# Kernel tuning notes

Hardware: AMD Instinct MI355X
Metric: run time of the kernel (lower is better)

## Reference

```python
import jax, jax.numpy as jnp
import numpy as np

ADAPTERS = 40   # adapter_num, hard-coded by range(40) and tsv 40x40
CAPS = 3        # num_capsules
CLASS_DIM = 200 # MAX_SEQ
IN_CH = CAPS * CLASS_DIM  # 600
B = 256
D = 768
NUM_ITERS = 3


def squash(v, axis=-1):
    sq = jnp.sum(v * v, axis=axis, keepdims=True)
    return (sq / (1.0 + sq)) * v / jnp.sqrt(sq)


def setup_inputs() -> dict:
    key = jax.random.key(0)
    k0, k1, k2, k3, k4 = jax.random.split(key, 5)
    x = jax.random.normal(k0, (B, ADAPTERS, IN_CH), jnp.float32)
    s = jax.random.uniform(k1, (1,), jnp.float32) * 4.0 + 1.0  # gate temperature
    route_weights = jax.random.normal(k2, (ADAPTERS, CAPS, IN_CH, CLASS_DIM), jnp.float32)
    larger_w = jax.random.normal(k3, (D, CAPS), jnp.float32) * 0.1  # Linear(3,768) weight [out,in]
    larger_b = jnp.zeros((D,), jnp.float32)
    elarger = jax.random.normal(k4, (ADAPTERS, D), jnp.float32)     # Embedding(40,768)
    tsv = jnp.tril(jnp.ones((ADAPTERS, ADAPTERS), jnp.float32))
    return {"t": 20, "x": x, "s": s, "route_weights": route_weights,
            "larger_w": larger_w, "larger_b": larger_b, "elarger": elarger, "tsv": tsv}


def reference(t, x, s, route_weights, larger_w, larger_b, elarger, tsv):
    bz = x.shape[0]
    # per-adapter small matmuls, batched: priors[n,b,k,d] = sum_c x[b,k,c] * W[k,n,c,d]
    priors = jnp.einsum('bkc,kncd->nbkd', x, route_weights)[:, :, :, None, :]  # [3,B,40,1,200]
    tsv_t = tsv[t]                                   # [40]
    mask = jnp.where(tsv_t == 0, -10000.0, 0.0)      # [40]
    tsv_b = tsv_t[None, None, :, None, None]
    mask_b = mask[None, None, :, None, None]
    logits = jnp.zeros_like(priors)
    vote = None
    for i in range(NUM_ITERS):
        logits = logits * tsv_b + mask_b
        probs = jax.nn.softmax(logits, axis=2)       # my_softmax over adapter dim
        vote = jnp.sum(probs * priors, axis=2, keepdims=True)   # [3,B,1,1,200]
        out = squash(vote, axis=-1)
        if i != NUM_ITERS - 1:
            logits = logits + jnp.sum(priors * out, axis=-1, keepdims=True)
    # torch's .view(bz, length, -1) on a [3,B,1,1,200] tensor: row-major reinterpretation
    h = vote.reshape(bz, CLASS_DIM, CAPS)            # [B,200,3]
    h = h @ larger_w.T + larger_b                    # [B,200,768]
    g = jax.nn.sigmoid(s * elarger[t])               # [768] (broadcast of [1]*[768])
    return h * g
```

## Files before the change

### kernel.cpp

```cpp
#include <hip/hip_runtime.h>
#include <hip/hip_bf16.h>

#define ADAPTERS 40
#define CAPS 3
#define IN_CH 600
#define BSZ 256
#define DCLS 200
#define DMODEL 768

typedef __attribute__((ext_vector_type(8))) short short8;
typedef __attribute__((ext_vector_type(4))) float f32x4;
typedef __attribute__((ext_vector_type(4))) float f4v;

#define RP 40
#define NCHUNK 19

__device__ __forceinline__ void split2(float f0, float f1,
                                       unsigned& hi, unsigned& lo) {
    unsigned u0 = __float_as_uint(f0), u1 = __float_as_uint(f1);
    unsigned h0 = u0 & 0xFFFF0000u, h1 = u1 & 0xFFFF0000u;
    hi = (u0 >> 16) | h1;
    float l0 = f0 - __uint_as_float(h0);
    float l1 = f1 - __uint_as_float(h1);
    lo = (__float_as_uint(l0) >> 16) | (__float_as_uint(l1) & 0xFFFF0000u);
}

__global__ __launch_bounds__(512) void k1_priors(
    const float* __restrict__ x,
    const float* __restrict__ rw,
    const float* __restrict__ tsv,
    const int* __restrict__ t_p,
    float* __restrict__ priors)
{
    int kk = blockIdx.z;
    int t = t_p[0];
    if (tsv[t * ADAPTERS + kk] == 0.0f) return;

    int b0 = blockIdx.x * 128;
    int j0 = blockIdx.y * 128;

    __shared__ __align__(16) unsigned short Ahi[128 * RP];
    __shared__ __align__(16) unsigned short Alo[128 * RP];
    __shared__ __align__(16) unsigned short Bhi[128 * RP];
    __shared__ __align__(16) unsigned short Blo[128 * RP];

    int tid = threadIdx.x;
    int lane = tid & 63, w = tid >> 6;
    int lm = lane & 15, lq = lane >> 4;
    int m0w = (w & 1) * 64;
    int n0w = (w >> 1) * 32;

    int a_bi = tid >> 2;
    int a_ci0 = (tid & 3) * 8;
    const float* a_row = x + ((size_t)(b0 + a_bi) * ADAPTERS + kk) * IN_CH;
    int b_jj = tid >> 2;
    int b_ci0 = (tid & 3) * 8;
    int j = j0 + b_jj;
    bool jvalid = (j < CAPS * DCLS);
    int cap = (j >= 2 * DCLS) ? 2 : ((j >= DCLS) ? 1 : 0);
    int d = j - cap * DCLS;
    const float* b_base = rw + ((size_t)(kk * 3 + cap) * IN_CH) * DCLS + d;

    f32x4 acc[4][2];
    #pragma unroll
    for (int mt = 0; mt < 4; mt++)
        #pragma unroll
        for (int nt = 0; nt < 2; nt++)
            acc[mt][nt] = (f32x4){0.f, 0.f, 0.f, 0.f};

    float4 ax[2];
    float  bx[8];

    {
        int c0 = 0;
        #pragma unroll
        for (int q = 0; q < 2; q++) {
            int c = c0 + a_ci0 + q * 4;
            ax[q] = (c + 4 <= IN_CH) ? *(const float4*)(a_row + c)
                                     : make_float4(0.f, 0.f, 0.f, 0.f);
        }
        #pragma unroll
        for (int i = 0; i < 8; i++) {
            int c = c0 + b_ci0 + i;
            bx[i] = (jvalid && c < IN_CH) ? b_base[(size_t)c * DCLS] : 0.f;
        }
    }

    for (int ch = 0; ch < NCHUNK; ch++) {
        unsigned ahi[4], alo[4], bhi[4], blo[4];
        split2(ax[0].x, ax[0].y, ahi[0], alo[0]);
        split2(ax[0].z, ax[0].w, ahi[1], alo[1]);
        split2(ax[1].x, ax[1].y, ahi[2], alo[2]);
        split2(ax[1].z, ax[1].w, ahi[3], alo[3]);
        #pragma unroll
        for (int p = 0; p < 4; p++)
            split2(bx[2 * p], bx[2 * p + 1], bhi[p], blo[p]);

        __syncthreads();
        {
            *(uint4*)((unsigned*)&Ahi[a_bi * RP + a_ci0]) =
                make_uint4(ahi[0], ahi[1], ahi[2], ahi[3]);
            *(uint4*)((unsigned*)&Alo[a_bi * RP + a_ci0]) =
                make_uint4(alo[0], alo[1], alo[2], alo[3]);
            *(uint4*)((unsigned*)&Bhi[b_jj * RP + b_ci0]) =
                make_uint4(bhi[0], bhi[1], bhi[2], bhi[3]);
            *(uint4*)((unsigned*)&Blo[b_jj * RP + b_ci0]) =
                make_uint4(blo[0], blo[1], blo[2], blo[3]);
        }
        __syncthreads();

        if (ch + 1 < NCHUNK) {
            int c0 = (ch + 1) * 32;
            #pragma unroll
            for (int q = 0; q < 2; q++) {
                int c = c0 + a_ci0 + q * 4;
                ax[q] = (c + 4 <= IN_CH) ? *(const float4*)(a_row + c)
                                         : make_float4(0.f, 0.f, 0.f, 0.f);
            }
            #pragma unroll
            for (int i = 0; i < 8; i++) {
                int c = c0 + b_ci0 + i;
                bx[i] = (jvalid && c < IN_CH) ? b_base[(size_t)c * DCLS] : 0.f;
            }
        }

        short8 Afh[4], Afl[4];
        #pragma unroll
        for (int mt = 0; mt < 4; mt++) {
            int row = m0w + mt * 16 + lm;
            Afh[mt] = *(const short8*)&Ahi[row * RP + lq * 8];
            Afl[mt] = *(const short8*)&Alo[row * RP + lq * 8];
        }
        #pragma unroll
        for (int nt = 0; nt < 2; nt++) {
            int row = n0w + nt * 16 + lm;
            short8 bh = *(const short8*)&Bhi[row * RP + lq * 8];
            short8 bl = *(const short8*)&Blo[row * RP + lq * 8];
            #pragma unroll
            for (int mt = 0; mt < 4; mt++) {
                acc[mt][nt] = __builtin_amdgcn_mfma_f32_16x16x32_bf16(
                    bh, Afh[mt], acc[mt][nt], 0, 0, 0);
                acc[mt][nt] = __builtin_amdgcn_mfma_f32_16x16x32_bf16(
                    bl, Afh[mt], acc[mt][nt], 0, 0, 0);
                acc[mt][nt] = __builtin_amdgcn_mfma_f32_16x16x32_bf16(
                    bh, Afl[mt], acc[mt][nt], 0, 0, 0);
            }
        }
    }

    #pragma unroll
    for (int nt = 0; nt < 2; nt++) {
        int jc = j0 + n0w + nt * 16 + lq * 4;
        if (jc >= CAPS * DCLS) continue;
        int capc = (jc >= 2 * DCLS) ? 2 : ((jc >= DCLS) ? 1 : 0);
        int dc = jc - capc * DCLS;
        #pragma unroll
        for (int mt = 0; mt < 4; mt++) {
            int b = b0 + m0w + mt * 16 + lm;
            float* dst = priors +
                ((size_t)(capc * BSZ + b) * ADAPTERS + kk) * DCLS + dc;
            *(f4v*)dst = *(f4v*)&acc[mt][nt];
        }
    }
}

__global__ __launch_bounds__(256) void k2_route(
    const float* __restrict__ priors,
    const float* __restrict__ tsv,
    const int* __restrict__ t_p,
    float* __restrict__ vote)
{
    int nb = blockIdx.x;
    int n = nb >> 8, b = nb & 255;
    int tid = threadIdx.x;
    int lane = tid & 63, wid = tid >> 6;

    __shared__ float Ps[ADAPTERS * DCLS];
    __shared__ float vout[DCLS];
    __shared__ float act[ADAPTERS];
    __shared__ float a_s[ADAPTERS];
    __shared__ float probs_s[ADAPTERS];
    __shared__ int   klist[ADAPTERS];
    __shared__ int   nact_s;
    __shared__ float red[4];
    __shared__ float scl;

    int t = t_p[0];
    if (tid < ADAPTERS) {
        act[tid] = tsv[t * ADAPTERS + tid];
        a_s[tid] = 0.0f;
    }
    __syncthreads();

    if (tid == 0) {
        int c = 0;
        for (int k = 0; k < ADAPTERS; k++)
            if (act[k] != 0.0f) klist[c++] = k;
        nact_s = c;
    }

    {
        const float4* pb4 = (const float4*)
            (priors + (size_t)(n * BSZ + b) * ADAPTERS * DCLS);
        float4* Ps4 = (float4*)Ps;
        for (int i4 = tid; i4 < ADAPTERS * (DCLS / 4); i4 += 256) {
            int k = i4 / (DCLS / 4);
            if (act[k] != 0.0f) Ps4[i4] = pb4[i4];
        }
    }
    __syncthreads();

    int nact = nact_s;
    float cnt = (float)nact;

    int td = tid;
    float v = 0.0f;
    if (td < DCLS) {
        for (int ki = 0; ki < nact; ki++)
            v += Ps[klist[ki] * DCLS + td];
        v /= cnt;
    }

    for (int it = 0; it < 3; it++) {
        if (it > 0) {
            if (wid == 0) {
                bool on = (lane < ADAPTERS) && (act[lane] != 0.f);
                float val = on ? a_s[lane] : -3.0e38f;
                float m = val;
                for (int off = 32; off; off >>= 1)
                    m = fmaxf(m, __shfl_down(m, off));
                m = __shfl(m, 0);
                float e = on ? expf(val - m) : 0.f;
                float ssum = e;
                for (int off = 32; off; off >>= 1)
                    ssum += __shfl_down(ssum, off);
                ssum = __shfl(ssum, 0);
                if (lane < ADAPTERS) probs_s[lane] = e / ssum;
            }
            __syncthreads();
            v = 0.0f;
            if (td < DCLS) {
                for (int ki = 0; ki < nact; ki++) {
                    int k = klist[ki];
                    v += probs_s[k] * Ps[k * DCLS + td];
                }
            }
        }
        if (it == 2) break;

        float vv = (td < DCLS) ? v * v : 0.f;
        for (int off = 32; off; off >>= 1) vv += __shfl_down(vv, off);
        if (lane == 0) red[wid] = vv;
        __syncthreads();
        if (tid == 0) {
            float sq = red[0] + red[1] + red[2] + red[3];
            scl = sqrtf(sq) / (1.0f + sq);
        }
        __syncthreads();
        if (td < DCLS) vout[td] = v * scl;
        __syncthreads();

        for (int ki = wid; ki < nact; ki += 4) {
            int k = klist[ki];
            const float* row = Ps + k * DCLS;
            float p = row[lane] * vout[lane]
                    + row[lane + 64] * vout[lane + 64]
                    + row[lane + 128] * vout[lane + 128];
            if (lane < DCLS - 192) p += row[lane + 192] * vout[lane + 192];
            for (int off = 32; off; off >>= 1) p += __shfl_down(p, off);
            if (lane == 0) a_s[k] += p;
        }
        __syncthreads();
    }

    if (td < DCLS) vote[(size_t)n * BSZ * DCLS + b * DCLS + td] = v;
}

__global__ __launch_bounds__(256) void k3_out(
    const float* __restrict__ vote,
    const float* __restrict__ s_p,
    const float* __restrict__ lw,
    const float* __restrict__ lb,
    const float* __restrict__ el,
    const int* __restrict__ t_p,
    float* __restrict__ out)
{
    __shared__ float vs[192];
    int tid = threadIdx.x;
    int r0 = blockIdx.x * 64;
    if (tid < 192) vs[tid] = vote[r0 * 3 + tid];

    int lane = tid & 63;
    int ty = tid >> 6;
    int j = blockIdx.y * 256 + lane * 4;

    int t = t_p[0];
    float s = s_p[0];
    float4 e4  = *(const float4*)(el + (size_t)t * DMODEL + j);
    float4 lb4 = *(const float4*)(lb + j);
    const float4* lw4 = (const float4*)(lw + (size_t)j * 3);
    float4 w0 = lw4[0], w1 = lw4[1], w2 = lw4[2];
    float ga = 1.0f / (1.0f + expf(-s * e4.x));
    float gb = 1.0f / (1.0f + expf(-s * e4.y));
    float gc = 1.0f / (1.0f + expf(-s * e4.z));
    float gd = 1.0f / (1.0f + expf(-s * e4.w));
    float4 g0 = make_float4(ga * w0.x, ga * w0.y, ga * w0.z, ga * lb4.x);
    float4 g1 = make_float4(gb * w0.w, gb * w1.x, gb * w1.y, gb * lb4.y);
    float4 g2 = make_float4(gc * w1.z, gc * w1.w, gc * w2.x, gc * lb4.z);
    float4 g3 = make_float4(gd * w2.y, gd * w2.z, gd * w2.w, gd * lb4.w);

    __syncthreads();

    #pragma unroll
    for (int it = 0; it < 16; it++) {
        int rl = it * 4 + ty;
        float h0 = vs[rl * 3 + 0];
        float h1 = vs[rl * 3 + 1];
        float h2 = vs[rl * 3 + 2];
        f4v o;
        o.x = h0 * g0.x + h1 * g0.y + h2 * g0.z + g0.w;
        o.y = h0 * g1.x + h1 * g1.y + h2 * g1.z + g1.w;
        o.z = h0 * g2.x + h1 * g2.y + h2 * g2.z + g2.w;
        o.w = h0 * g3.x + h1 * g3.y + h2 * g3.z + g3.w;
        __builtin_nontemporal_store(o, (f4v*)(out + (size_t)(r0 + rl) * DMODEL + j));
    }
}

extern "C" void kernel_launch(void* const* d_in, const int* in_sizes, int n_in,
                              void* d_out, int out_size, void* d_ws, size_t ws_size,
                              hipStream_t stream) {
    const int*   t   = (const int*)d_in[0];
    const float* x   = (const float*)d_in[1];
    const float* s   = (const float*)d_in[2];
    const float* rw  = (const float*)d_in[3];
    const float* lw  = (const float*)d_in[4];
    const float* lb  = (const float*)d_in[5];
    const float* el  = (const float*)d_in[6];
    const float* tsv = (const float*)d_in[7];
    float* out = (float*)d_out;

    char* wsb = (char*)d_ws;
    float* priors = (float*)wsb;
    float* vote   = (float*)(wsb + 24576000);

    k1_priors<<<dim3(2, 5, ADAPTERS), dim3(512), 0, stream>>>(x, rw, tsv, t, priors);
    k2_route<<<dim3(CAPS * BSZ), dim3(256), 0, stream>>>(priors, tsv, t, vote);
    k3_out<<<dim3(BSZ * DCLS / 64, 3), dim3(256), 0, stream>>>(vote, s, lw, lb, el, t, out);
}
```

Baseline: 282.6 us.

## Double-buffer LDS tiles in priors GEMM to drop one barrier per chunk

Makes the split-bf16 A/B shared-memory tiles double-buffered in the priors kernel. Each iteration reads fragments from the current buffer, writes the next chunk's split data into the other buffer, and issues global loads two chunks ahead. This leaves one __syncthreads per chunk instead of two and lets LDS writes and global loads overlap the MFMA work. Shared memory per block doubles to about 80 KB, which may limit blocks per CU, and register pressure rises.

```diff
diff --git a/kernel.cpp b/kernel.cpp
--- a/kernel.cpp
+++ b/kernel.cpp
@@ -39,10 +39,10 @@
     int b0 = blockIdx.x * 128;
     int j0 = blockIdx.y * 128;
 
-    __shared__ __align__(16) unsigned short Ahi[128 * RP];
-    __shared__ __align__(16) unsigned short Alo[128 * RP];
-    __shared__ __align__(16) unsigned short Bhi[128 * RP];
-    __shared__ __align__(16) unsigned short Blo[128 * RP];
+    __shared__ __align__(16) unsigned short Ahi[2][128 * RP];
+    __shared__ __align__(16) unsigned short Alo[2][128 * RP];
+    __shared__ __align__(16) unsigned short Bhi[2][128 * RP];
+    __shared__ __align__(16) unsigned short Blo[2][128 * RP];
 
     int tid = threadIdx.x;
     int lane = tid & 63, w = tid >> 6;
@@ -71,8 +71,8 @@
     float4 ax[2];
     float  bx[8];
 
-    {
-        int c0 = 0;
+    auto load_regs = [&](int ch) {
+        int c0 = ch * 32;
         #pragma unroll
         for (int q = 0; q < 2; q++) {
             int c = c0 + a_ci0 + q * 4;
@@ -84,9 +84,9 @@
             int c = c0 + b_ci0 + i;
             bx[i] = (jvalid && c < IN_CH) ? b_base[(size_t)c * DCLS] : 0.f;
         }
-    }
-
-    for (int ch = 0; ch < NCHUNK; ch++) {
+    };
+
+    auto split_write = [&](int buf) {
         unsigned ahi[4], alo[4], bhi[4], blo[4];
         split2(ax[0].x, ax[0].y, ahi[0], alo[0]);
         split2(ax[0].z, ax[0].w, ahi[1], alo[1]);
@@ -95,57 +95,56 @@
         #pragma unroll
         for (int p = 0; p < 4; p++)
             split2(bx[2 * p], bx[2 * p + 1], bhi[p], blo[p]);
-
-        __syncthreads();
-        {
-            *(uint4*)((unsigned*)&Ahi[a_bi * RP + a_ci0]) =
-                make_uint4(ahi[0], ahi[1], ahi[2], ahi[3]);
-            *(uint4*)((unsigned*)&Alo[a_bi * RP + a_ci0]) =
-                make_uint4(alo[0], alo[1], alo[2], alo[3]);
-            *(uint4*)((unsigned*)&Bhi[b_jj * RP + b_ci0]) =
-                make_uint4(bhi[0], bhi[1], bhi[2], bhi[3]);
-            *(uint4*)((unsigned*)&Blo[b_jj * RP + b_ci0]) =
-                make_uint4(blo[0], blo[1], blo[2], blo[3]);
-        }
-        __syncthreads();
-
-        if (ch + 1 < NCHUNK) {
-            int c0 = (ch + 1) * 32;
-            #pragma unroll
-            for (int q = 0; q < 2; q++) {
-                int c = c0 + a_ci0 + q * 4;
-                ax[q] = (c + 4 <= IN_CH) ? *(const float4*)(a_row + c)
-                                         : make_float4(0.f, 0.f, 0.f, 0.f);
-            }
-            #pragma unroll
-            for (int i = 0; i < 8; i++) {
-                int c = c0 + b_ci0 + i;
-                bx[i] = (jvalid && c < IN_CH) ? b_base[(size_t)c * DCLS] : 0.f;
-            }
-        }
-
-        short8 Afh[4], Afl[4];
+        *(uint4*)((unsigned*)&Ahi[buf][a_bi * RP + a_ci0]) =
+            make_uint4(ahi[0], ahi[1], ahi[2], ahi[3]);
+        *(uint4*)((unsigned*)&Alo[buf][a_bi * RP + a_ci0]) =
+            make_uint4(alo[0], alo[1], alo[2], alo[3]);
+        *(uint4*)((unsigned*)&Bhi[buf][b_jj * RP + b_ci0]) =
+            make_uint4(bhi[0], bhi[1], bhi[2], bhi[3]);
+        *(uint4*)((unsigned*)&Blo[buf][b_jj * RP + b_ci0]) =
+            make_uint4(blo[0], blo[1], blo[2], blo[3]);
+    };
+
+    load_regs(0);
+    split_write(0);
+    load_regs(1);
+    __syncthreads();
+
+    for (int ch = 0; ch < NCHUNK; ch++) {
+        int cb = ch & 1;
+
+        short8 Afh[4], Afl[4], Bfh[2], Bfl[2];
         #pragma unroll
         for (int mt = 0; mt < 4; mt++) {
             int row = m0w + mt * 16 + lm;
-            Afh[mt] = *(const short8*)&Ahi[row * RP + lq * 8];
-            Afl[mt] = *(const short8*)&Alo[row * RP + lq * 8];
+            Afh[mt] = *(const short8*)&Ahi[cb][row * RP + lq * 8];
+            Afl[mt] = *(const short8*)&Alo[cb][row * RP + lq * 8];
         }
         #pragma unroll
         for (int nt = 0; nt < 2; nt++) {
             int row = n0w + nt * 16 + lm;
-            short8 bh = *(const short8*)&Bhi[row * RP + lq * 8];
-            short8 bl = *(const short8*)&Blo[row * RP + lq * 8];
+            Bfh[nt] = *(const short8*)&Bhi[cb][row * RP + lq * 8];
+            Bfl[nt] = *(const short8*)&Blo[cb][row * RP + lq * 8];
+        }
+
+        if (ch + 1 < NCHUNK) {
+            split_write(cb ^ 1);
+            if (ch + 2 < NCHUNK) load_regs(ch + 2);
+        }
+
+        #pragma unroll
+        for (int nt = 0; nt < 2; nt++) {
             #pragma unroll
             for (int mt = 0; mt < 4; mt++) {
                 acc[mt][nt] = __builtin_amdgcn_mfma_f32_16x16x32_bf16(
-                    bh, Afh[mt], acc[mt][nt], 0, 0, 0);
+                    Bfh[nt], Afh[mt], acc[mt][nt], 0, 0, 0);
                 acc[mt][nt] = __builtin_amdgcn_mfma_f32_16x16x32_bf16(
-                    bl, Afh[mt], acc[mt][nt], 0, 0, 0);
+                    Bfl[nt], Afh[mt], acc[mt][nt], 0, 0, 0);
                 acc[mt][nt] = __builtin_amdgcn_mfma_f32_16x16x32_bf16(
-                    bh, Afl[mt], acc[mt][nt], 0, 0, 0);
+                    Bfh[nt], Afl[mt], acc[mt][nt], 0, 0, 0);
             }
         }
+        __syncthreads();
     }
 
     #pragma unroll
```

Result: faster. 272.1 us (median of 2 runs) (-3.7%).
